# Kernel optimization log

Measured on AMD Instinct MI355X. Metric: run time of the kernel, lower is better.

The kernel has to match this reference:

```python
import jax, jax.numpy as jnp
import numpy as np

N_NODES = 50000
N_EDGES = 800000
IN_CH = 128
OUT_CH = 32
HEADS = 8
NEG_SLOPE = 0.2


def setup_inputs() -> dict:
    key = jax.random.key(0)
    k1, k2, k3, k4, k5, k6 = jax.random.split(key, 6)
    x = jax.random.normal(k1, (N_NODES, IN_CH), dtype=jnp.float32)
    edge_index = jax.random.randint(k2, (2, N_EDGES), 0, N_NODES, dtype=jnp.int64)
    # Glorot-ish scaled params
    W = jax.random.normal(k3, (IN_CH, HEADS * OUT_CH), dtype=jnp.float32) * (1.0 / np.sqrt(IN_CH))
    att_src = jax.random.normal(k4, (HEADS, OUT_CH), dtype=jnp.float32) * (1.0 / np.sqrt(OUT_CH))
    att_dst = jax.random.normal(k5, (HEADS, OUT_CH), dtype=jnp.float32) * (1.0 / np.sqrt(OUT_CH))
    bias = jax.random.normal(k6, (HEADS * OUT_CH,), dtype=jnp.float32) * 0.01
    return {"x": x, "edge_index": edge_index, "W": W, "att_src": att_src, "att_dst": att_dst, "bias": bias}


def reference(x, edge_index, W, att_src, att_dst, bias):
    N = x.shape[0]
    # PyG GATConv default: add self loops
    loops = jnp.arange(N, dtype=edge_index.dtype)
    src = jnp.concatenate([edge_index[0], loops])  # message source j
    dst = jnp.concatenate([edge_index[1], loops])  # message destination i

    # Linear projection: [N, H, C]
    h = (x @ W).reshape(N, HEADS, OUT_CH)

    # Per-node attention logits per head: [N, H]
    a_src = jnp.einsum('nhc,hc->nh', h, att_src)
    a_dst = jnp.einsum('nhc,hc->nh', h, att_dst)

    # Per-edge scores: [E, H]
    e = jax.nn.leaky_relu(a_src[src] + a_dst[dst], NEG_SLOPE)

    # Segment softmax over edges sharing a destination (self loops guarantee non-empty segments)
    e_max = jax.ops.segment_max(e, dst, num_segments=N)
    e_exp = jnp.exp(e - e_max[dst])
    e_sum = jax.ops.segment_sum(e_exp, dst, num_segments=N)
    alpha = e_exp / (e_sum[dst] + 1e-16)  # [E, H]

    # Weighted message aggregation: [N, H, C] -> concat heads [N, H*C]
    msg = h[src] * alpha[:, :, None]
    out = jax.ops.segment_sum(msg, dst, num_segments=N).reshape(N, HEADS * OUT_CH)
    out = out + bias
    # unlinear = ReLU (act='relu', norm=None)
    return jax.nn.relu(out)
```

## Files before the change

### kernel.cpp

```cpp
#include <hip/hip_runtime.h>

#define IN_CH 128
#define OUT_CH 32
#define HEADS 8
#define HC 256
#define NEG_SLOPE 0.2f

typedef __attribute__((ext_vector_type(8))) short short8;
typedef __attribute__((ext_vector_type(4))) float f32x4;

__device__ __forceinline__ float bflo(unsigned u) { return __uint_as_float(u << 16); }
__device__ __forceinline__ float bfhi(unsigned u) { return __uint_as_float(u & 0xffff0000u); }
__device__ __forceinline__ float bf2f(unsigned short u) { return __uint_as_float(((unsigned)u) << 16); }
__device__ __forceinline__ unsigned short f2bf(float f) {
    unsigned u = __float_as_uint(f);
    u = (u + 0x7fffu + ((u >> 16) & 1u)) >> 16;
    return (unsigned short)u;
}

__global__ __launch_bounds__(256)
void gat_prep(const float* __restrict__ W, unsigned short* __restrict__ Wt,
              int* __restrict__ counts, int n)
{
    const int idx = blockIdx.x * 256 + threadIdx.x;
    const int k = idx >> 8;
    const int col = idx & 255;
    Wt[col * IN_CH + k] = f2bf(W[idx]);
    for (int i = idx; i < n; i += 32768) counts[i] = 0;
}

__global__ __launch_bounds__(256)
void gat_proj_mfma(const float* __restrict__ x, const unsigned short* __restrict__ Wt,
                   const float* __restrict__ attS, const float* __restrict__ attD,
                   unsigned short* __restrict__ h, float* __restrict__ aS,
                   float* __restrict__ aD, int N)
{
    __shared__ unsigned short lbuf[32 * 264];

    const int tid = threadIdx.x;
    const int lane = tid & 63;
    const int w = tid >> 6;
    const int row0 = blockIdx.x * 32;

    short8 bfr[4][4];
    {
        const unsigned short* wp = Wt + (size_t)(w * 64 + (lane & 15)) * IN_CH
                                      + ((lane >> 4) << 3);
#pragma unroll
        for (int i = 0; i < 4; ++i)
#pragma unroll
            for (int ks = 0; ks < 4; ++ks)
                bfr[ks][i] = *(const short8*)(wp + i * 16 * IN_CH + ks * 32);
    }

#pragma unroll
    for (int u = 0; u < 2; ++u) {
        const int unit = tid + u * 256;
        const int srow = unit >> 4;
        const int sseg = unit & 15;
        const int grow = row0 + srow;
        float4 v0 = make_float4(0.f, 0.f, 0.f, 0.f), v1 = v0;
        if (grow < N) {
            const float* xp = x + (size_t)grow * IN_CH + sseg * 8;
            v0 = *(const float4*)xp;
            v1 = *(const float4*)(xp + 4);
        }
        short8 pk;
        pk[0] = (short)f2bf(v0.x); pk[1] = (short)f2bf(v0.y);
        pk[2] = (short)f2bf(v0.z); pk[3] = (short)f2bf(v0.w);
        pk[4] = (short)f2bf(v1.x); pk[5] = (short)f2bf(v1.y);
        pk[6] = (short)f2bf(v1.z); pk[7] = (short)f2bf(v1.w);
        *(short8*)&lbuf[srow * 136 + sseg * 8] = pk;
    }
    __syncthreads();

    f32x4 acc[2][4];
#pragma unroll
    for (int m = 0; m < 2; ++m)
#pragma unroll
        for (int i = 0; i < 4; ++i) acc[m][i] = (f32x4){0.f, 0.f, 0.f, 0.f};

#pragma unroll
    for (int ks = 0; ks < 4; ++ks) {
#pragma unroll
        for (int m = 0; m < 2; ++m) {
            const short8 a = *(const short8*)&lbuf[((lane & 15) + m * 16) * 136
                                                   + ks * 32 + ((lane >> 4) << 3)];
#pragma unroll
            for (int i = 0; i < 4; ++i)
                acc[m][i] = __builtin_amdgcn_mfma_f32_16x16x32_bf16(a, bfr[ks][i], acc[m][i], 0, 0, 0);
        }
    }

    const int rbase = (lane >> 4) << 2;
    float ps[2][2][4], pd[2][2][4];
#pragma unroll
    for (int m = 0; m < 2; ++m)
#pragma unroll
        for (int hp = 0; hp < 2; ++hp)
#pragma unroll
            for (int r = 0; r < 4; ++r) { ps[m][hp][r] = 0.f; pd[m][hp][r] = 0.f; }

#pragma unroll
    for (int i = 0; i < 4; ++i) {
        const int hp = i >> 1;
        const float asv = attS[(w * 2 + hp) * 32 + (i & 1) * 16 + (lane & 15)];
        const float adv = attD[(w * 2 + hp) * 32 + (i & 1) * 16 + (lane & 15)];
#pragma unroll
        for (int m = 0; m < 2; ++m)
#pragma unroll
            for (int r = 0; r < 4; ++r) {
                ps[m][hp][r] = fmaf(acc[m][i][r], asv, ps[m][hp][r]);
                pd[m][hp][r] = fmaf(acc[m][i][r], adv, pd[m][hp][r]);
            }
    }
#pragma unroll
    for (int off = 1; off < 16; off <<= 1) {
#pragma unroll
        for (int m = 0; m < 2; ++m)
#pragma unroll
            for (int hp = 0; hp < 2; ++hp)
#pragma unroll
                for (int r = 0; r < 4; ++r) {
                    ps[m][hp][r] += __shfl_xor(ps[m][hp][r], off, 64);
                    pd[m][hp][r] += __shfl_xor(pd[m][hp][r], off, 64);
                }
    }
    if ((lane & 15) == 0) {
#pragma unroll
        for (int m = 0; m < 2; ++m)
#pragma unroll
            for (int hp = 0; hp < 2; ++hp)
#pragma unroll
                for (int r = 0; r < 4; ++r) {
                    const int grow = row0 + m * 16 + rbase + r;
                    if (grow < N) {
                        aS[grow * HEADS + w * 2 + hp] = ps[m][hp][r];
                        aD[grow * HEADS + w * 2 + hp] = pd[m][hp][r];
                    }
                }
    }

    __syncthreads();
#pragma unroll
    for (int i = 0; i < 4; ++i) {
        const int col = w * 64 + i * 16 + (lane & 15);
#pragma unroll
        for (int m = 0; m < 2; ++m)
#pragma unroll
            for (int r = 0; r < 4; ++r)
                lbuf[(m * 16 + rbase + r) * 264 + col] = f2bf(acc[m][i][r]);
    }
    __syncthreads();

#pragma unroll
    for (int u = 0; u < 4; ++u) {
        const int unit = u * 256 + tid;
        const int srow = unit >> 5;
        const int sseg = unit & 31;
        const int grow = row0 + srow;
        if (grow < N)
            *(short8*)(h + (size_t)grow * HC + sseg * 8) =
                *(const short8*)&lbuf[srow * 264 + sseg * 8];
    }
}

__global__ __launch_bounds__(256)
void gat_hist(const int* __restrict__ dst, int* __restrict__ counts,
              int* __restrict__ rank, int E)
{
    int i = (blockIdx.x * 256 + threadIdx.x) * 8;
    if (i + 7 < E) {
        const int4 d0 = *(const int4*)&dst[i];
        const int4 d1 = *(const int4*)&dst[i + 4];
        int4 r0, r1;
        r0.x = atomicAdd(&counts[d0.x], 1);
        r0.y = atomicAdd(&counts[d0.y], 1);
        r0.z = atomicAdd(&counts[d0.z], 1);
        r0.w = atomicAdd(&counts[d0.w], 1);
        r1.x = atomicAdd(&counts[d1.x], 1);
        r1.y = atomicAdd(&counts[d1.y], 1);
        r1.z = atomicAdd(&counts[d1.z], 1);
        r1.w = atomicAdd(&counts[d1.w], 1);
        *(int4*)&rank[i] = r0;
        *(int4*)&rank[i + 4] = r1;
    } else {
        for (; i < E; ++i) rank[i] = atomicAdd(&counts[dst[i]], 1);
    }
}

__global__ __launch_bounds__(256)
void gat_scan1(const int* __restrict__ counts, int* __restrict__ bsum, int n)
{
    __shared__ int ws[4];
    const int t = threadIdx.x;
    const int lane = t & 63;
    const int wid = t >> 6;
    const int idx = blockIdx.x * 1024 + t * 4;
    int4 v = {0, 0, 0, 0};
    if (idx + 3 < n) v = *(const int4*)&counts[idx];
    else {
        if (idx < n)     v.x = counts[idx];
        if (idx + 1 < n) v.y = counts[idx + 1];
        if (idx + 2 < n) v.z = counts[idx + 2];
    }
    int s4 = v.x + v.y + v.z + v.w;
#pragma unroll
    for (int off = 1; off < 64; off <<= 1) s4 += __shfl_xor(s4, off, 64);
    if (lane == 0) ws[wid] = s4;
    __syncthreads();
    if (t == 0) bsum[blockIdx.x] = ws[0] + ws[1] + ws[2] + ws[3];
}

__global__ __launch_bounds__(256)
void gat_scan3(const int* __restrict__ counts, const int* __restrict__ bsum,
               int* __restrict__ offsets, int n, int nb, int E)
{
    __shared__ int wsums[4];
    __shared__ int bbase_s;
    const int t = threadIdx.x;
    const int lane = t & 63;
    const int wid = t >> 6;

    if (t < 64) {
        const int v = (t < nb) ? bsum[t] : 0;
        int inc = v;
#pragma unroll
        for (int off = 1; off < 64; off <<= 1) {
            const int y = __shfl_up(inc, off, 64);
            if (t >= off) inc += y;
        }
        const int myv   = __shfl(v, blockIdx.x, 64);
        const int myinc = __shfl(inc, blockIdx.x, 64);
        if (t == 0) bbase_s = myinc - myv;
    }

    const int idx = blockIdx.x * 1024 + t * 4;
    int4 v = {0, 0, 0, 0};
    if (idx + 3 < n) v = *(const int4*)&counts[idx];
    else {
        if (idx < n)     v.x = counts[idx];
        if (idx + 1 < n) v.y = counts[idx + 1];
        if (idx + 2 < n) v.z = counts[idx + 2];
    }
    const int s4 = v.x + v.y + v.z + v.w;
    int inc = s4;
#pragma unroll
    for (int off = 1; off < 64; off <<= 1) {
        const int y = __shfl_up(inc, off, 64);
        if (lane >= off) inc += y;
    }
    if (lane == 63) wsums[wid] = inc;
    __syncthreads();
    int wbase = 0;
    for (int i = 0; i < wid; ++i) wbase += wsums[i];
    const int base = bbase_s + wbase + (inc - s4);
    int4 o;
    o.x = base;
    o.y = base + v.x;
    o.z = o.y + v.y;
    o.w = o.z + v.z;
    if (idx + 3 < n) {
        *(int4*)&offsets[idx] = o;
    } else {
        if (idx < n)     offsets[idx] = o.x;
        if (idx + 1 < n) offsets[idx + 1] = o.y;
        if (idx + 2 < n) offsets[idx + 2] = o.z;
    }
    if (blockIdx.x == 0 && t == 0) offsets[n] = E;
}

__global__ __launch_bounds__(256)
void gat_scatter(const int* __restrict__ src, const int* __restrict__ dst,
                 const int* __restrict__ rank, const int* __restrict__ offsets,
                 int* __restrict__ ssrc, unsigned short* __restrict__ ealpha,
                 const float* __restrict__ aS, const float* __restrict__ aD, int E)
{
    const int e = blockIdx.x * 256 + threadIdx.x;
    if (e >= E) return;
    const int s = src[e];
    const int d = dst[e];
    const int pos = offsets[d] + rank[e];
    ssrc[pos] = s;
    const float4 s0 = *(const float4*)(aS + (size_t)s * HEADS);
    const float4 s1 = *(const float4*)(aS + (size_t)s * HEADS + 4);
    const float4 d0 = *(const float4*)(aD + (size_t)d * HEADS);
    const float4 d1 = *(const float4*)(aD + (size_t)d * HEADS + 4);
    float lg[8] = { s0.x + d0.x, s0.y + d0.y, s0.z + d0.z, s0.w + d0.w,
                    s1.x + d1.x, s1.y + d1.y, s1.z + d1.z, s1.w + d1.w };
    short8 al;
#pragma unroll
    for (int k = 0; k < 8; ++k) {
        const float v = lg[k] > 0.f ? lg[k] : NEG_SLOPE * lg[k];
        al[k] = (short)f2bf(__expf(v));
    }
    *(short8*)(ealpha + (size_t)pos * HEADS) = al;
}

__global__ __launch_bounds__(256)
void gat_agg(const unsigned short* __restrict__ h,
             const float* __restrict__ aS, const float* __restrict__ aD,
             const int* __restrict__ offsets, const int* __restrict__ ssrc,
             const unsigned short* __restrict__ ealpha,
             const float* __restrict__ bias, float* __restrict__ out, int N)
{
    const int t = threadIdx.x;
    const int lane = t & 63;
    const int node = blockIdx.x * 4 + (t >> 6);
    if (node >= N) return;

    const int half = lane >> 5;
    const int hl = lane & 31;
    const int head = hl >> 2;
    const int ch = head * 32 + (hl & 3) * 8;

    float sum;
    float acc[8];
    {
        float lg0 = aS[node * HEADS + head] + aD[node * HEADS + head];
        lg0 = (lg0 > 0.f) ? lg0 : NEG_SLOPE * lg0;
        const float w0 = half ? 0.f : __expf(lg0);
        sum = w0;
        const uint4 hv = *(const uint4*)(h + (size_t)node * HC + ch);
        acc[0] = w0 * bflo(hv.x); acc[1] = w0 * bfhi(hv.x);
        acc[2] = w0 * bflo(hv.y); acc[3] = w0 * bfhi(hv.y);
        acc[4] = w0 * bflo(hv.z); acc[5] = w0 * bfhi(hv.z);
        acc[6] = w0 * bflo(hv.w); acc[7] = w0 * bfhi(hv.w);
    }

    const int beg = offsets[node];
    const int end = offsets[node + 1];
    const int last = end - 1;

    int sE[4];
    float aE[4];
#pragma unroll
    for (int j = 0; j < 4; ++j) { sE[j] = node; aE[j] = 0.f; }

    if (beg < end) {
#pragma unroll
        for (int j = 0; j < 4; ++j) {
            const int e = beg + half * 4 + j;
            const int c = min(e, last);
            int s = ssrc[c];
            float a = bf2f(ealpha[(size_t)c * HEADS + head]);
            if (e > last) { s = node; a = 0.f; }
            sE[j] = s; aE[j] = a;
        }
    }

    for (int base = beg; base < end; base += 8) {
        int tS[4]; float tA[4];
#pragma unroll
        for (int j = 0; j < 4; ++j) {
            const int e = base + 8 + half * 4 + j;
            const int c = min(e, last);
            int s = ssrc[c];
            float a = bf2f(ealpha[(size_t)c * HEADS + head]);
            if (e > last) { s = node; a = 0.f; }
            tS[j] = s; tA[j] = a;
        }
        uint4 v[4];
#pragma unroll
        for (int j = 0; j < 4; ++j)
            v[j] = *(const uint4*)(h + (size_t)sE[j] * HC + ch);
#pragma unroll
        for (int j = 0; j < 4; ++j) {
            const float a = aE[j];
            sum += a;
            acc[0] = fmaf(a, bflo(v[j].x), acc[0]);
            acc[1] = fmaf(a, bfhi(v[j].x), acc[1]);
            acc[2] = fmaf(a, bflo(v[j].y), acc[2]);
            acc[3] = fmaf(a, bfhi(v[j].y), acc[3]);
            acc[4] = fmaf(a, bflo(v[j].z), acc[4]);
            acc[5] = fmaf(a, bfhi(v[j].z), acc[5]);
            acc[6] = fmaf(a, bflo(v[j].w), acc[6]);
            acc[7] = fmaf(a, bfhi(v[j].w), acc[7]);
        }
#pragma unroll
        for (int j = 0; j < 4; ++j) { sE[j] = tS[j]; aE[j] = tA[j]; }
    }

#pragma unroll
    for (int j = 0; j < 8; ++j) acc[j] += __shfl_xor(acc[j], 32, 64);
    sum += __shfl_xor(sum, 32, 64);

    const float inv = 1.f / (sum + 1e-16f);
    const int cbase = ch + half * 4;
    const int j0 = half * 4;
    const float4 bv = *(const float4*)(bias + cbase);
    float4 o;
    o.x = fmaxf(fmaf(acc[j0 + 0], inv, bv.x), 0.f);
    o.y = fmaxf(fmaf(acc[j0 + 1], inv, bv.y), 0.f);
    o.z = fmaxf(fmaf(acc[j0 + 2], inv, bv.z), 0.f);
    o.w = fmaxf(fmaf(acc[j0 + 3], inv, bv.w), 0.f);
    *(float4*)(out + (size_t)node * HC + cbase) = o;
}

extern "C" void kernel_launch(void* const* d_in, const int* in_sizes, int n_in,
                              void* d_out, int out_size, void* d_ws, size_t ws_size,
                              hipStream_t stream)
{
    const float* x    = (const float*)d_in[0];
    const int*   ei   = (const int*)d_in[1];
    const float* W    = (const float*)d_in[2];
    const float* attS = (const float*)d_in[3];
    const float* attD = (const float*)d_in[4];
    const float* bias = (const float*)d_in[5];
    float* out = (float*)d_out;

    const int N = in_sizes[0] / IN_CH;
    const int E = in_sizes[1] / 2;
    const int* esrc = ei;
    const int* edst = ei + E;

    unsigned short* h = (unsigned short*)d_ws;
    float* aS = (float*)(h + (size_t)N * HC);
    float* aD = aS + (size_t)N * HEADS;
    int* counts  = (int*)(aD + (size_t)N * HEADS);
    int* offsets = counts + N;
    int* rank    = offsets + (N + 4);
    int* ssrc    = rank + E;
    int* bsum    = ssrc + E;
    unsigned short* Wt = (unsigned short*)(bsum + 64);
    unsigned short* ealpha = Wt + IN_CH * HC;

    const int nb = (N + 1023) / 1024;

    gat_prep<<<(IN_CH * HC) / 256, 256, 0, stream>>>(W, Wt, counts, N);
    gat_proj_mfma<<<(N + 31) / 32, 256, 0, stream>>>(x, Wt, attS, attD, h, aS, aD, N);
    gat_hist<<<(E / 8 + 255) / 256, 256, 0, stream>>>(edst, counts, rank, E);
    gat_scan1<<<nb, 256, 0, stream>>>(counts, bsum, N);
    gat_scan3<<<nb, 256, 0, stream>>>(counts, bsum, offsets, N, nb, E);
    gat_scatter<<<(E + 255) / 256, 256, 0, stream>>>(esrc, edst, rank, offsets, ssrc, ealpha, aS, aD, E);
    gat_agg<<<(N + 3) / 4, 256, 0, stream>>>(h, aS, aD, offsets, ssrc, ealpha, bias, out, N);
}
```

Before: 177.3 us.

## Merge projection and degree histogram into one launch, drop weight prep kernel

Fuses the projection GEMM and the destination histogram into a single grid, with extra blocks dedicated to the atomic histogram, so the two independent stages overlap and one launch disappears. The separate weight transpose/convert kernel is removed: each projection block now reads fp32 W directly with strided loads and converts to bf16 in registers, and counts are zeroed with a memset instead. This trades launch overhead and a dependency for redundant, uncoalesced W reads in every projection block.

```diff
diff --git a/kernel.cpp b/kernel.cpp
--- a/kernel.cpp
+++ b/kernel.cpp
@@ -19,38 +19,58 @@
 }
 
 __global__ __launch_bounds__(256)
-void gat_prep(const float* __restrict__ W, unsigned short* __restrict__ Wt,
-              int* __restrict__ counts, int n)
-{
-    const int idx = blockIdx.x * 256 + threadIdx.x;
-    const int k = idx >> 8;
-    const int col = idx & 255;
-    Wt[col * IN_CH + k] = f2bf(W[idx]);
-    for (int i = idx; i < n; i += 32768) counts[i] = 0;
-}
-
-__global__ __launch_bounds__(256)
-void gat_proj_mfma(const float* __restrict__ x, const unsigned short* __restrict__ Wt,
-                   const float* __restrict__ attS, const float* __restrict__ attD,
-                   unsigned short* __restrict__ h, float* __restrict__ aS,
-                   float* __restrict__ aD, int N)
+void gat_projhist(const float* __restrict__ x, const float* __restrict__ W,
+                  const float* __restrict__ attS, const float* __restrict__ attD,
+                  unsigned short* __restrict__ h, float* __restrict__ aS,
+                  float* __restrict__ aD, int N,
+                  const int* __restrict__ dst, int* __restrict__ counts,
+                  int* __restrict__ rank, int E, int projBlocks)
 {
     __shared__ unsigned short lbuf[32 * 264];
 
     const int tid = threadIdx.x;
+
+    if ((int)blockIdx.x >= projBlocks) {
+        const int hb = blockIdx.x - projBlocks;
+        int i = (hb * 256 + tid) * 8;
+        if (i + 7 < E) {
+            const int4 d0 = *(const int4*)&dst[i];
+            const int4 d1 = *(const int4*)&dst[i + 4];
+            int4 r0, r1;
+            r0.x = atomicAdd(&counts[d0.x], 1);
+            r0.y = atomicAdd(&counts[d0.y], 1);
+            r0.z = atomicAdd(&counts[d0.z], 1);
+            r0.w = atomicAdd(&counts[d0.w], 1);
+            r1.x = atomicAdd(&counts[d1.x], 1);
+            r1.y = atomicAdd(&counts[d1.y], 1);
+            r1.z = atomicAdd(&counts[d1.z], 1);
+            r1.w = atomicAdd(&counts[d1.w], 1);
+            *(int4*)&rank[i] = r0;
+            *(int4*)&rank[i + 4] = r1;
+        } else {
+            for (; i < E; ++i) rank[i] = atomicAdd(&counts[dst[i]], 1);
+        }
+        return;
+    }
+
     const int lane = tid & 63;
     const int w = tid >> 6;
     const int row0 = blockIdx.x * 32;
 
     short8 bfr[4][4];
     {
-        const unsigned short* wp = Wt + (size_t)(w * 64 + (lane & 15)) * IN_CH
-                                      + ((lane >> 4) << 3);
+        const int colb = w * 64 + (lane & 15);
+        const int k0 = (lane >> 4) << 3;
 #pragma unroll
         for (int i = 0; i < 4; ++i)
 #pragma unroll
-            for (int ks = 0; ks < 4; ++ks)
-                bfr[ks][i] = *(const short8*)(wp + i * 16 * IN_CH + ks * 32);
+            for (int ks = 0; ks < 4; ++ks) {
+                short8 b;
+#pragma unroll
+                for (int j = 0; j < 8; ++j)
+                    b[j] = (short)f2bf(W[(size_t)(ks * 32 + k0 + j) * HC + colb + i * 16]);
+                bfr[ks][i] = b;
+            }
     }
 
 #pragma unroll
@@ -162,30 +182,6 @@
         if (grow < N)
             *(short8*)(h + (size_t)grow * HC + sseg * 8) =
                 *(const short8*)&lbuf[srow * 264 + sseg * 8];
-    }
-}
-
-__global__ __launch_bounds__(256)
-void gat_hist(const int* __restrict__ dst, int* __restrict__ counts,
-              int* __restrict__ rank, int E)
-{
-    int i = (blockIdx.x * 256 + threadIdx.x) * 8;
-    if (i + 7 < E) {
-        const int4 d0 = *(const int4*)&dst[i];
-        const int4 d1 = *(const int4*)&dst[i + 4];
-        int4 r0, r1;
-        r0.x = atomicAdd(&counts[d0.x], 1);
-        r0.y = atomicAdd(&counts[d0.y], 1);
-        r0.z = atomicAdd(&counts[d0.z], 1);
-        r0.w = atomicAdd(&counts[d0.w], 1);
-        r1.x = atomicAdd(&counts[d1.x], 1);
-        r1.y = atomicAdd(&counts[d1.y], 1);
-        r1.z = atomicAdd(&counts[d1.z], 1);
-        r1.w = atomicAdd(&counts[d1.w], 1);
-        *(int4*)&rank[i] = r0;
-        *(int4*)&rank[i + 4] = r1;
-    } else {
-        for (; i < E; ++i) rank[i] = atomicAdd(&counts[dst[i]], 1);
     }
 }
 
@@ -422,14 +418,15 @@
     int* rank    = offsets + (N + 4);
     int* ssrc    = rank + E;
     int* bsum    = ssrc + E;
-    unsigned short* Wt = (unsigned short*)(bsum + 64);
-    unsigned short* ealpha = Wt + IN_CH * HC;
+    unsigned short* ealpha = (unsigned short*)(bsum + 64);
 
     const int nb = (N + 1023) / 1024;
-
-    gat_prep<<<(IN_CH * HC) / 256, 256, 0, stream>>>(W, Wt, counts, N);
-    gat_proj_mfma<<<(N + 31) / 32, 256, 0, stream>>>(x, Wt, attS, attD, h, aS, aD, N);
-    gat_hist<<<(E / 8 + 255) / 256, 256, 0, stream>>>(edst, counts, rank, E);
+    const int projBlocks = (N + 31) / 32;
+    const int histBlocks = (E / 8 + 255) / 256;
+
+    hipMemsetAsync(counts, 0, (size_t)N * sizeof(int), stream);
+    gat_projhist<<<projBlocks + histBlocks, 256, 0, stream>>>(
+        x, W, attS, attD, h, aS, aD, N, edst, counts, rank, E, projBlocks);
     gat_scan1<<<nb, 256, 0, stream>>>(counts, bsum, N);
     gat_scan3<<<nb, 256, 0, stream>>>(counts, bsum, offsets, N, nb, E);
     gat_scatter<<<(E + 255) / 256, 256, 0, stream>>>(esrc, edst, rank, offsets, ssrc, ealpha, aS, aD, E);
```

Result: no change. 176.2 us (-0.6%).
